# Kernel optimization log

Hardware: AMD Instinct MI355X
Metric: run time of the kernel (lower is better)

## Reference

```python
import jax, jax.numpy as jnp
import numpy as np

N, E, B = 100000, 3200000, 1024
D_LM, K, H, C, L = 1024, 128, 256, 40, 2
T = 0.1
LN_EPS = 1e-5


def _layernorm(x, g, b):
    m = x.mean(-1, keepdims=True)
    v = ((x - m) ** 2).mean(-1, keepdims=True)
    return (x - m) * jax.lax.rsqrt(v + LN_EPS) * g + b


def _gcn_conv(x, W, b, src, dst, norm, self_w):
    h = x @ W
    agg = jax.ops.segment_sum(h[src] * norm[:, None], dst, num_segments=N)
    return agg + h * self_w[:, None] + b


def setup_inputs() -> dict:
    key = jax.random.key(0)
    ks = jax.random.split(key, 20)
    s = 0.02
    rn = lambda k, shp: jax.random.normal(k, shp, jnp.float32) * s
    return {
        "hidden_embeds": jax.random.normal(ks[0], (L, N, D_LM), jnp.float32),
        "proj_W1": rn(ks[1], (L, D_LM, K)),
        "proj_b1": jnp.zeros((L, K), jnp.float32),
        "ln_g": jnp.ones((L, K), jnp.float32),
        "ln_b": jnp.zeros((L, K), jnp.float32),
        "proj_W2": rn(ks[2], (L, K, K)),
        "proj_b2": jnp.zeros((L, K), jnp.float32),
        "alphas": jnp.zeros((L,), jnp.float32),
        "gcn_W1": rn(ks[3], (L, K, H)),
        "gcn_b1": jnp.zeros((L, H), jnp.float32),
        "gcn_W2": rn(ks[4], (L, H, K)),
        "gcn_b2": jnp.zeros((L, K), jnp.float32),
        "clf_W": rn(ks[5], (2 * K, C)),
        "clf_b": jnp.zeros((C,), jnp.float32),
        "edge_index": jax.random.randint(ks[6], (2, E), 0, N, jnp.int64 if jax.config.jax_enable_x64 else jnp.int32),
        "mapping": jax.random.randint(ks[7], (B,), 0, N, jnp.int64 if jax.config.jax_enable_x64 else jnp.int32),
    }


def reference(hidden_embeds, proj_W1, proj_b1, ln_g, ln_b, proj_W2, proj_b2,
              alphas, gcn_W1, gcn_b1, gcn_W2, gcn_b2, clf_W, clf_b,
              edge_index, mapping):
    src, dst = edge_index[0], edge_index[1]
    ones = jnp.ones((E,), jnp.float32)
    # GCN normalization (self loops included): deg over dst + 1
    deg = jax.ops.segment_sum(ones, dst, num_segments=N) + 1.0
    dis = jax.lax.rsqrt(deg)
    norm = dis[src] * dis[dst]          # per-edge D^-1/2 A D^-1/2
    self_w = 1.0 / deg                  # self-loop weight dis[i]*dis[i]

    last = None
    for i in range(L):
        # projector: Linear -> LayerNorm -> ReLU -> Linear
        h = hidden_embeds[i] @ proj_W1[i] + proj_b1[i]
        h = jax.nn.relu(_layernorm(h, ln_g[i], ln_b[i]))
        h = h @ proj_W2[i] + proj_b2[i]
        if i > 0:
            a = jax.nn.sigmoid(alphas[i] / T)
            h = h * a + last * (1.0 - a)
        # 2-layer GCN encoder (dropout=0)
        z = jax.nn.relu(_gcn_conv(h, gcn_W1[i], gcn_b1[i], src, dst, norm, self_w))
        last = _gcn_conv(z, gcn_W2[i], gcn_b2[i], src, dst, norm, self_w)

    # custom_global_mean_pool: mean over {node} U {out-neighbors} U {in-neighbors}
    sum_n = (jax.ops.segment_sum(last[dst], src, num_segments=N)
             + jax.ops.segment_sum(last[src], dst, num_segments=N))
    cnt = (jax.ops.segment_sum(ones, src, num_segments=N)
           + jax.ops.segment_sum(ones, dst, num_segments=N))
    pooled = (last[mapping] + sum_n[mapping]) / (1.0 + cnt[mapping])[:, None]

    out = jnp.concatenate([last[mapping], pooled], axis=1)  # [B, 2K]
    return out @ clf_W + clf_b
```

## Files before the change

### kernel.cpp

```cpp
#include <hip/hip_runtime.h>
#include <hip/hip_bf16.h>
#include <math.h>

using short8 = __attribute__((ext_vector_type(8))) short;
using f32x4  = __attribute__((ext_vector_type(4))) float;

#define PSTRIDE 2048

__device__ __forceinline__ short f2bf(float f) {
    __hip_bfloat16 h = __float2bfloat16(f);
    return *reinterpret_cast<short*>(&h);
}
__device__ __forceinline__ float bf2f(unsigned short u) {
    return __uint_as_float(((unsigned)u) << 16);
}


__global__ void map_scatter_k(const int* __restrict__ mapping, int* __restrict__ map_idx, int B)
{
    int b = blockIdx.x * blockDim.x + threadIdx.x;
    if (b < B) map_idx[mapping[b]] = b;
}

__launch_bounds__(1024)
__global__ void bin_count_k(const int* __restrict__ dst, int E, int* __restrict__ bin_cnt)
{
    __shared__ int h[4096];
    for (int i = threadIdx.x; i < 4096; i += 1024) h[i] = 0;
    __syncthreads();
    int base = blockIdx.x * 32768;
#pragma unroll
    for (int i = 0; i < 32; ++i) {
        int e = base + i * 1024 + threadIdx.x;
        if (e < E) atomicAdd(&h[dst[e] >> 5], 1);
    }
    __syncthreads();
    for (int i = threadIdx.x; i < 4096; i += 1024) {
        int c = h[i];
        if (c) atomicAdd(&bin_cnt[i], c);
    }
}

__launch_bounds__(1024)
__global__ void scan_bins_k(const int* __restrict__ cnt, int* __restrict__ off,
                            int* __restrict__ cur)
{
    __shared__ int wsum[16];
    int tid = threadIdx.x, lane = tid & 63, wid = tid >> 6;
    int4 v = ((const int4*)cnt)[tid];
    int s0 = v.x, s1 = s0 + v.y, s2 = s1 + v.z, s3 = s2 + v.w;
    int q = s3;
#pragma unroll
    for (int o = 1; o < 64; o <<= 1) { int t = __shfl_up(q, o); if (lane >= o) q += t; }
    if (lane == 63) wsum[wid] = q;
    __syncthreads();
    if (wid == 0) {
        int w = (lane < 16) ? wsum[lane] : 0;
#pragma unroll
        for (int o = 1; o < 16; o <<= 1) { int t = __shfl_up(w, o); if (lane >= o) w += t; }
        if (lane < 16) wsum[lane] = w;
    }
    __syncthreads();
    int base = (wid ? wsum[wid - 1] : 0) + q - s3;
    int4 o4; o4.x = base; o4.y = base + s0; o4.z = base + s1; o4.w = base + s2;
    ((int4*)off)[tid] = o4;
    ((int4*)cur)[tid] = o4;
    if (tid == 1023) off[4096] = base + s3;
}

__launch_bounds__(256)
__global__ void bin_scatter_k(const int* __restrict__ ei, int E,
                              const int* __restrict__ map_idx,
                              int* __restrict__ bin_cur, unsigned* __restrict__ pairs,
                              int* __restrict__ pcnt, int* __restrict__ pnb)
{
    int e = blockIdx.x * blockDim.x + threadIdx.x;
    if (e >= E) return;
    int s = ei[e];
    int d = ei[E + e];
    int p = atomicAdd(&bin_cur[d >> 5], 1);
    pairs[p] = (unsigned)s | ((unsigned)(d & 31) << 27);
    int ms = map_idx[s];
    if (ms >= 0) {
        int i = atomicAdd(&pcnt[ms], 1);
        if (i < PSTRIDE) pnb[ms * PSTRIDE + i] = d;
    }
    int md = map_idx[d];
    if (md >= 0) {
        int i = atomicAdd(&pcnt[md], 1);
        if (i < PSTRIDE) pnb[md * PSTRIDE + i] = s;
    }
}

__launch_bounds__(256)
__global__ void bin_csr_k(const unsigned* __restrict__ pairs, const int* __restrict__ bin_off,
                          int* __restrict__ csr_in, int* __restrict__ in_off,
                          float* __restrict__ dis, int N)
{
    __shared__ int lcnt[32];
    __shared__ int lofs[32];
    __shared__ int lcur[32];
    int b = blockIdx.x;
    int tid = threadIdx.x;
    if (tid < 32) lcnt[tid] = 0;
    __syncthreads();
    int beg = bin_off[b], end = bin_off[b + 1];
    for (int i = beg + tid; i < end; i += 256)
        atomicAdd(&lcnt[pairs[i] >> 27], 1);
    __syncthreads();
    if (tid == 0) {
        int run = beg;
#pragma unroll
        for (int j = 0; j < 32; ++j) { lofs[j] = run; lcur[j] = run; run += lcnt[j]; }
    }
    __syncthreads();
    int n0 = b * 32;
    if (tid < 32 && n0 + tid < N) {
        in_off[n0 + tid] = lofs[tid];
        float dg = (float)lcnt[tid] + 1.0f;
        dis[n0 + tid] = rsqrtf(dg);
    }
    if (b == gridDim.x - 1 && tid == 0) in_off[N] = end;
    for (int i = beg + tid; i < end; i += 256) {
        unsigned pr = pairs[i];
        int p = atomicAdd(&lcur[pr >> 27], 1);
        csr_in[p] = (int)(pr & 0x07FFFFFFu);
    }
}

__global__ void transpose_wb_k(const float* __restrict__ src, short* __restrict__ dst,
                               int LAY, int R, int Cc)
{
    int idx = blockIdx.x * blockDim.x + threadIdx.x;
    int tot = LAY * R * Cc;
    if (idx >= tot) return;
    int lay = idx / (R * Cc);
    int rem = idx - lay * R * Cc;
    int r = rem / Cc;
    int c = rem - r * Cc;
    dst[(size_t)lay * R * Cc + (size_t)c * R + r] = f2bf(src[idx]);
}

__launch_bounds__(256)
__global__ void proj_fused_k(const float* __restrict__ X,
                             const short* __restrict__ W1t,
                             const float* __restrict__ b1,
                             const float* __restrict__ lng,
                             const float* __restrict__ lnb,
                             const short* __restrict__ W2t,
                             const float* __restrict__ b2,
                             const float* __restrict__ alphas, int layer,
                             const unsigned short* __restrict__ last,
                             const float* __restrict__ dis,
                             short* __restrict__ out, int nrows)
{
    __shared__ short S[26624];

    const int tid  = threadIdx.x;
    const int lane = tid & 63;
    const int wave = tid >> 6;
    const int wr   = wave >> 1;
    const int wc   = wave & 1;
    const int g    = lane >> 4;
    const int lr   = lane & 15;
    const int row0 = blockIdx.x * 128;

    f32x4 acc[4][4];
#pragma unroll
    for (int fr = 0; fr < 4; ++fr)
#pragma unroll
        for (int fc = 0; fc < 4; ++fc) acc[fr][fc] = (f32x4){0.f, 0.f, 0.f, 0.f};

    const int xr   = tid >> 1;
    const int xc0  = (tid & 1) * 32;
    const bool xvalid = (row0 + xr) < nrows;
    const float* xbase = X + (size_t)(row0 + xr) * 1024 + xc0;
    const short* wbase = W1t + (size_t)(tid >> 1) * 1024 + (tid & 1) * 32;

    float4 xv[8];
    short8 wv[4];
    if (xvalid) {
#pragma unroll
        for (int m = 0; m < 8; ++m) xv[m] = *(const float4*)&xbase[m * 4];
    } else {
#pragma unroll
        for (int m = 0; m < 8; ++m) xv[m] = make_float4(0.f, 0.f, 0.f, 0.f);
    }
#pragma unroll
    for (int m = 0; m < 4; ++m) wv[m] = *(const short8*)&wbase[m * 8];

    for (int k0 = 0; k0 < 1024; k0 += 64) {
#pragma unroll
        for (int m = 0; m < 4; ++m) {
            short8 p;
            p[0]=f2bf(xv[2*m].x); p[1]=f2bf(xv[2*m].y); p[2]=f2bf(xv[2*m].z); p[3]=f2bf(xv[2*m].w);
            p[4]=f2bf(xv[2*m+1].x); p[5]=f2bf(xv[2*m+1].y); p[6]=f2bf(xv[2*m+1].z); p[7]=f2bf(xv[2*m+1].w);
            *(short8*)&S[xr * 72 + xc0 + m * 8] = p;
        }
#pragma unroll
        for (int m = 0; m < 4; ++m)
            *(short8*)&S[9216 + (tid >> 1) * 72 + (tid & 1) * 32 + m * 8] = wv[m];
        __syncthreads();

        if (k0 + 64 < 1024) {
            if (xvalid) {
                const float* xp = xbase + k0 + 64;
#pragma unroll
                for (int m = 0; m < 8; ++m) xv[m] = *(const float4*)&xp[m * 4];
            }
            const short* wp = wbase + k0 + 64;
#pragma unroll
            for (int m = 0; m < 4; ++m) wv[m] = *(const short8*)&wp[m * 8];
        }

#pragma unroll
        for (int kk = 0; kk < 64; kk += 32) {
            short8 a[4], b[4];
#pragma unroll
            for (int fr = 0; fr < 4; ++fr)
                a[fr] = *(short8*)&S[(wr * 64 + fr * 16 + lr) * 72 + kk + g * 8];
#pragma unroll
            for (int fc = 0; fc < 4; ++fc)
                b[fc] = *(short8*)&S[9216 + (wc * 64 + fc * 16 + lr) * 72 + kk + g * 8];
#pragma unroll
            for (int fr = 0; fr < 4; ++fr)
#pragma unroll
                for (int fc = 0; fc < 4; ++fc)
                    acc[fr][fc] = __builtin_amdgcn_mfma_f32_16x16x32_bf16(a[fr], b[fc], acc[fr][fc], 0, 0, 0);
        }
        __syncthreads();
    }

    float* P = (float*)&S[17408];
    {
        float b1v[4], gv[4], bv[4];
#pragma unroll
        for (int fc = 0; fc < 4; ++fc) {
            int col = wc * 64 + fc * 16 + lr;
            b1v[fc] = b1[col]; gv[fc] = lng[col]; bv[fc] = lnb[col];
        }
#pragma unroll
        for (int fr = 0; fr < 4; ++fr) {
#pragma unroll
            for (int j = 0; j < 4; ++j) {
                float s = 0.f, q = 0.f;
#pragma unroll
                for (int fc = 0; fc < 4; ++fc) {
                    float t = acc[fr][fc][j] + b1v[fc];
                    acc[fr][fc][j] = t;
                    s += t; q += t * t;
                }
#pragma unroll
                for (int m = 1; m < 16; m <<= 1) {
                    s += __shfl_xor(s, m);
                    q += __shfl_xor(q, m);
                }
                if (lr == 0) {
                    int row = wr * 64 + fr * 16 + 4 * g + j;
                    P[row * 4 + wc * 2]     = s;
                    P[row * 4 + wc * 2 + 1] = q;
                }
            }
        }
        __syncthreads();
#pragma unroll
        for (int fr = 0; fr < 4; ++fr) {
#pragma unroll
            for (int j = 0; j < 4; ++j) {
                int row = wr * 64 + fr * 16 + 4 * g + j;
                float s = P[row * 4 + 0] + P[row * 4 + 2];
                float q = P[row * 4 + 1] + P[row * 4 + 3];
                float mean = s * (1.0f / 128.0f);
                float var  = q * (1.0f / 128.0f) - mean * mean;
                float inv  = rsqrtf(var + 1e-5f);
#pragma unroll
                for (int fc = 0; fc < 4; ++fc) {
                    float h = fmaxf((acc[fr][fc][j] - mean) * inv * gv[fc] + bv[fc], 0.f);
                    S[row * 136 + wc * 64 + fc * 16 + lr] = f2bf(h);
                }
            }
        }
    }
    __syncthreads();

    f32x4 acc2[4][4];
#pragma unroll
    for (int fr = 0; fr < 4; ++fr)
#pragma unroll
        for (int fc = 0; fc < 4; ++fc) acc2[fr][fc] = (f32x4){0.f, 0.f, 0.f, 0.f};

    for (int k0 = 0; k0 < 128; k0 += 64) {
        {
            int c  = tid >> 1;
            int kb = (tid & 1) * 32;
            const short* wp = W2t + (size_t)c * 128 + k0 + kb;
#pragma unroll
            for (int m = 0; m < 4; ++m)
                *(short8*)&S[17408 + c * 72 + kb + m * 8] = *(const short8*)&wp[m * 8];
        }
        __syncthreads();
#pragma unroll
        for (int kk = 0; kk < 64; kk += 32) {
            short8 a[4], b[4];
#pragma unroll
            for (int fr = 0; fr < 4; ++fr)
                a[fr] = *(short8*)&S[(wr * 64 + fr * 16 + lr) * 136 + k0 + kk + g * 8];
#pragma unroll
            for (int fc = 0; fc < 4; ++fc)
                b[fc] = *(short8*)&S[17408 + (wc * 64 + fc * 16 + lr) * 72 + kk + g * 8];
#pragma unroll
            for (int fr = 0; fr < 4; ++fr)
#pragma unroll
                for (int fc = 0; fc < 4; ++fc)
                    acc2[fr][fc] = __builtin_amdgcn_mfma_f32_16x16x32_bf16(a[fr], b[fc], acc2[fr][fc], 0, 0, 0);
        }
        __syncthreads();
    }

    float b2v[4];
#pragma unroll
    for (int fc = 0; fc < 4; ++fc) b2v[fc] = b2[wc * 64 + fc * 16 + lr];
    float asig = 0.f, omas = 0.f;
    if (last) {
        float al = alphas[layer];
        asig = 1.0f / (1.0f + expf(-al * 10.0f));
        omas = 1.0f - asig;
    }
#pragma unroll
    for (int fr = 0; fr < 4; ++fr) {
#pragma unroll
        for (int j = 0; j < 4; ++j) {
            int gr = row0 + wr * 64 + fr * 16 + 4 * g + j;
            if (gr >= nrows) continue;
            float disr = dis[gr];
#pragma unroll
            for (int fc = 0; fc < 4; ++fc) {
                int col = wc * 64 + fc * 16 + lr;
                float o = acc2[fr][fc][j] + b2v[fc];
                if (last) o = asig * o + omas * bf2f(last[(size_t)gr * 128 + col]);
                out[(size_t)gr * 128 + col] = f2bf(o * disr);
            }
        }
    }
}

__launch_bounds__(256)
__global__ void gcn_mlp_k(const short* __restrict__ U,
                          const short* __restrict__ W1t,
                          const float* __restrict__ gb1,
                          const short* __restrict__ W2t,
                          const float* __restrict__ dis,
                          short* __restrict__ V, int M)
{
    __shared__ short S[35840];

    const int tid  = threadIdx.x;
    const int lane = tid & 63;
    const int wave = tid >> 6;
    const int g    = lane >> 4;
    const int lr   = lane & 15;
    const int m0   = blockIdx.x * 64;

#pragma unroll
    for (int it = 0; it < 4; ++it) {
        int i = tid + it * 256;
        int r = i >> 4;
        int c8 = i & 15;
        short8 v = {0,0,0,0,0,0,0,0};
        int gr = m0 + r;
        if (gr < M) v = *(const short8*)&U[(size_t)gr * 128 + c8 * 8];
        *(short8*)&S[r * 136 + c8 * 8] = v;
    }

    f32x4 acc[4][4];
#pragma unroll
    for (int fr = 0; fr < 4; ++fr)
#pragma unroll
        for (int fc = 0; fc < 4; ++fc) acc[fr][fc] = (f32x4){0.f, 0.f, 0.f, 0.f};

    for (int k0 = 0; k0 < 128; k0 += 64) {
#pragma unroll
        for (int it = 0; it < 8; ++it) {
            int i = tid + it * 256;
            int r = i >> 3;
            int c8 = i & 7;
            *(short8*)&S[17408 + r * 72 + c8 * 8] =
                *(const short8*)&W1t[(size_t)r * 128 + k0 + c8 * 8];
        }
        __syncthreads();
#pragma unroll
        for (int kk = 0; kk < 64; kk += 32) {
            short8 a[4], b[4];
#pragma unroll
            for (int fr = 0; fr < 4; ++fr)
                a[fr] = *(short8*)&S[(fr * 16 + lr) * 136 + k0 + kk + g * 8];
#pragma unroll
            for (int fc = 0; fc < 4; ++fc)
                b[fc] = *(short8*)&S[17408 + (wave * 64 + fc * 16 + lr) * 72 + kk + g * 8];
#pragma unroll
            for (int fr = 0; fr < 4; ++fr)
#pragma unroll
                for (int fc = 0; fc < 4; ++fc)
                    acc[fr][fc] = __builtin_amdgcn_mfma_f32_16x16x32_bf16(a[fr], b[fc], acc[fr][fc], 0, 0, 0);
        }
        __syncthreads();
    }

    {
        float bb[4];
#pragma unroll
        for (int fc = 0; fc < 4; ++fc) bb[fc] = gb1[wave * 64 + fc * 16 + lr];
#pragma unroll
        for (int fr = 0; fr < 4; ++fr) {
#pragma unroll
            for (int j = 0; j < 4; ++j) {
                int rloc = fr * 16 + 4 * g + j;
#pragma unroll
                for (int fc = 0; fc < 4; ++fc) {
                    float zv = fmaxf(acc[fr][fc][j] + bb[fc], 0.f);
                    S[rloc * 264 + wave * 64 + fc * 16 + lr] = f2bf(zv);
                }
            }
        }
    }

    f32x4 acc2[4][2];
#pragma unroll
    for (int fr = 0; fr < 4; ++fr) {
        acc2[fr][0] = (f32x4){0.f, 0.f, 0.f, 0.f};
        acc2[fr][1] = (f32x4){0.f, 0.f, 0.f, 0.f};
    }

    for (int k0 = 0; k0 < 256; k0 += 64) {
#pragma unroll
        for (int it = 0; it < 4; ++it) {
            int i = tid + it * 256;
            int r = i >> 3;
            int c8 = i & 7;
            *(short8*)&S[16896 + r * 72 + c8 * 8] =
                *(const short8*)&W2t[(size_t)r * 256 + k0 + c8 * 8];
        }
        __syncthreads();
#pragma unroll
        for (int kk = 0; kk < 64; kk += 32) {
            short8 a[4], b[2];
#pragma unroll
            for (int fr = 0; fr < 4; ++fr)
                a[fr] = *(short8*)&S[(fr * 16 + lr) * 264 + k0 + kk + g * 8];
#pragma unroll
            for (int fc = 0; fc < 2; ++fc)
                b[fc] = *(short8*)&S[16896 + (wave * 32 + fc * 16 + lr) * 72 + kk + g * 8];
#pragma unroll
            for (int fr = 0; fr < 4; ++fr)
#pragma unroll
                for (int fc = 0; fc < 2; ++fc)
                    acc2[fr][fc] = __builtin_amdgcn_mfma_f32_16x16x32_bf16(a[fr], b[fc], acc2[fr][fc], 0, 0, 0);
        }
        __syncthreads();
    }

#pragma unroll
    for (int fr = 0; fr < 4; ++fr) {
#pragma unroll
        for (int j = 0; j < 4; ++j) {
            int gr = m0 + fr * 16 + 4 * g + j;
            if (gr >= M) continue;
            float disr = dis[gr];
#pragma unroll
            for (int fc = 0; fc < 2; ++fc)
                V[(size_t)gr * 128 + wave * 32 + fc * 16 + lr] = f2bf(acc2[fr][fc][j] * disr);
        }
    }
}

__launch_bounds__(256)
__global__ void agg_k(const unsigned* __restrict__ x, unsigned* __restrict__ y,
                      const int* __restrict__ off, const int* __restrict__ csr,
                      const float* __restrict__ dis,
                      const float* __restrict__ bias, int N)
{
    int node = __builtin_amdgcn_readfirstlane(blockIdx.x * 4 + (threadIdx.x >> 6));
    if (node >= N) return;
    int lane = threadIdx.x & 63;
    int beg = off[node], end = off[node + 1];

    float ax0 = 0.f, ay0 = 0.f, ax1 = 0.f, ay1 = 0.f;
    float ax2 = 0.f, ay2 = 0.f, ax3 = 0.f, ay3 = 0.f;
    int e = beg;
    for (; e + 4 <= end; e += 4) {
        int s0 = csr[e], s1 = csr[e + 1], s2 = csr[e + 2], s3 = csr[e + 3];
        unsigned v0 = x[(size_t)s0 * 64 + lane];
        unsigned v1 = x[(size_t)s1 * 64 + lane];
        unsigned v2 = x[(size_t)s2 * 64 + lane];
        unsigned v3 = x[(size_t)s3 * 64 + lane];
        ax0 += __uint_as_float(v0 << 16);
        ay0 += __uint_as_float(v0 & 0xFFFF0000u);
        ax1 += __uint_as_float(v1 << 16);
        ay1 += __uint_as_float(v1 & 0xFFFF0000u);
        ax2 += __uint_as_float(v2 << 16);
        ay2 += __uint_as_float(v2 & 0xFFFF0000u);
        ax3 += __uint_as_float(v3 << 16);
        ay3 += __uint_as_float(v3 & 0xFFFF0000u);
    }
    for (; e < end; ++e) {
        int s = csr[e];
        unsigned v = x[(size_t)s * 64 + lane];
        ax0 += __uint_as_float(v << 16);
        ay0 += __uint_as_float(v & 0xFFFF0000u);
    }
    unsigned vo = x[(size_t)node * 64 + lane];
    float accx = ((ax0 + ax1) + (ax2 + ax3)) + __uint_as_float(vo << 16);
    float accy = ((ay0 + ay1) + (ay2 + ay3)) + __uint_as_float(vo & 0xFFFF0000u);

    float dn = dis[node];
    float rx = dn * accx;
    float ry = dn * accy;
    if (bias) { rx += bias[lane * 2]; ry += bias[lane * 2 + 1]; }
    unsigned p = (unsigned)(unsigned short)f2bf(rx) | ((unsigned)(unsigned short)f2bf(ry) << 16);
    y[(size_t)node * 64 + lane] = p;
}

__launch_bounds__(128)
__global__ void pool_clf_k(const unsigned short* __restrict__ last,
                           const int* __restrict__ mapping,
                           const int* __restrict__ map_idx,
                           const int* __restrict__ pcnt, const int* __restrict__ pnb,
                           const float* __restrict__ clfW, const float* __restrict__ clfb,
                           float* __restrict__ out, int C)
{
    int b = blockIdx.x;
    int tid = threadIdx.x;
    int n = mapping[b];
    int rep = map_idx[n];
    int cnt = pcnt[rep];
    int m = cnt < PSTRIDE ? cnt : PSTRIDE;

    float s = 0.f;
    const int* nb = pnb + (size_t)rep * PSTRIDE;
    for (int i = 0; i < m; ++i)
        s += bf2f(last[(size_t)nb[i] * 128 + tid]);

    float lv = bf2f(last[(size_t)n * 128 + tid]);
    float pooled = (lv + s) / (1.0f + (float)cnt);

    __shared__ float feat[256];
    feat[tid] = lv;
    feat[128 + tid] = pooled;
    __syncthreads();

    for (int c = tid; c < C; c += blockDim.x) {
        float o = clfb[c];
        for (int j = 0; j < 256; ++j) o = fmaf(feat[j], clfW[j * C + c], o);
        out[(size_t)b * C + c] = o;
    }
}

extern "C" void kernel_launch(void* const* d_in, const int* in_sizes, int n_in,
                              void* d_out, int out_size, void* d_ws, size_t ws_size,
                              hipStream_t stream)
{
    const float* hidden = (const float*)d_in[0];
    const float* pW1    = (const float*)d_in[1];
    const float* pb1    = (const float*)d_in[2];
    const float* lng    = (const float*)d_in[3];
    const float* lnb    = (const float*)d_in[4];
    const float* pW2    = (const float*)d_in[5];
    const float* pb2    = (const float*)d_in[6];
    const float* alphas = (const float*)d_in[7];
    const float* gW1    = (const float*)d_in[8];
    const float* gb1    = (const float*)d_in[9];
    const float* gW2    = (const float*)d_in[10];
    const float* gb2    = (const float*)d_in[11];
    const float* clfW   = (const float*)d_in[12];
    const float* clfb   = (const float*)d_in[13];
    const int*   ei     = (const int*)d_in[14];
    const int*   mapping= (const int*)d_in[15];

    const int L   = in_sizes[7];
    const int K   = in_sizes[2] / L;
    const int H   = in_sizes[9] / L;
    const int C   = in_sizes[13];
    const int DLM = in_sizes[1] / (L * K);
    const int N   = in_sizes[0] / (L * DLM);
    const int E   = in_sizes[14] / 2;
    const int B   = in_sizes[15];
    const int NBINS = (N + 31) / 32;

    char* ws = (char*)d_ws;
    size_t off = 0;
    auto carve = [&](size_t bytes) -> char* {
        char* p = ws + off;
        off += (bytes + 255) & ~(size_t)255;
        return p;
    };
    int*      map_idx = (int*)carve((size_t)N * 4);
    int*      pcnt    = (int*)carve((size_t)B * 4);
    int*      pnb     = (int*)carve((size_t)B * PSTRIDE * 4);
    int*      bin_cnt = (int*)carve(4096 * 4);
    int*      bin_off = (int*)carve(4097 * 4);
    int*      bin_cur = (int*)carve(4096 * 4);
    unsigned* pairs   = (unsigned*)carve((size_t)E * 4);
    int*      in_off  = (int*)carve((size_t)(N + 1) * 4);
    float*    dis     = (float*)carve((size_t)N * 4);
    int*      csr_in  = (int*)carve((size_t)E * 4);
    short*    bufA    = (short*)carve((size_t)N * K * 2);
    short*    bufU    = (short*)carve((size_t)N * K * 2);
    short*    bufLast = (short*)carve((size_t)N * K * 2);
    short*    w1t     = (short*)carve((size_t)L * K * DLM * 2);
    short*    w2t     = (short*)carve((size_t)L * K * K * 2);
    short*    gw1t    = (short*)carve((size_t)L * H * K * 2);
    short*    gw2t    = (short*)carve((size_t)L * K * H * 2);
    (void)ws_size; (void)n_in; (void)out_size;

    hipMemsetAsync(bin_cnt, 0, 4096 * 4, stream);
    hipMemsetAsync(map_idx, 0xFF, (size_t)N * 4, stream);
    hipMemsetAsync(pcnt, 0, (size_t)B * 4, stream);
    map_scatter_k<<<dim3((B + 255) / 256), 256, 0, stream>>>(mapping, map_idx, B);
    bin_count_k<<<dim3((E + 32767) / 32768), 1024, 0, stream>>>(ei + E, E, bin_cnt);
    scan_bins_k<<<dim3(1), 1024, 0, stream>>>(bin_cnt, bin_off, bin_cur);
    bin_scatter_k<<<dim3((E + 255) / 256), 256, 0, stream>>>(ei, E, map_idx, bin_cur,
                                                             pairs, pcnt, pnb);
    bin_csr_k<<<dim3(NBINS), 256, 0, stream>>>(pairs, bin_off, csr_in, in_off,
                                               dis, N);

    transpose_wb_k<<<dim3((L * DLM * K + 255) / 256), 256, 0, stream>>>(pW1, w1t, L, DLM, K);
    transpose_wb_k<<<dim3((L * K * K + 255) / 256), 256, 0, stream>>>(pW2, w2t, L, K, K);
    transpose_wb_k<<<dim3((L * K * H + 255) / 256), 256, 0, stream>>>(gW1, gw1t, L, K, H);
    transpose_wb_k<<<dim3((L * H * K + 255) / 256), 256, 0, stream>>>(gW2, gw2t, L, H, K);

    const int nblk64  = (N + 63) / 64;
    const int nblk128 = (N + 127) / 128;

    for (int i = 0; i < L; ++i) {
        proj_fused_k<<<dim3(nblk128), 256, 0, stream>>>(
            hidden + (size_t)i * N * DLM,
            w1t + (size_t)i * K * DLM,
            pb1 + (size_t)i * K,
            lng + (size_t)i * K,
            lnb + (size_t)i * K,
            w2t + (size_t)i * K * K,
            pb2 + (size_t)i * K,
            alphas, i,
            (i > 0) ? (const unsigned short*)bufLast : nullptr,
            dis,
            bufA, N);

        agg_k<<<dim3((N + 3) / 4), 256, 0, stream>>>(
            (const unsigned*)bufA, (unsigned*)bufU, in_off, csr_in, dis, nullptr, N);
        gcn_mlp_k<<<dim3(nblk64), 256, 0, stream>>>(
            bufU, gw1t + (size_t)i * H * K, gb1 + (size_t)i * H,
            gw2t + (size_t)i * K * H, dis, bufA, N);
        agg_k<<<dim3((N + 3) / 4), 256, 0, stream>>>(
            (const unsigned*)bufA, (unsigned*)bufLast, in_off, csr_in, dis,
            gb2 + (size_t)i * K, N);
    }

    pool_clf_k<<<dim3(B), 128, 0, stream>>>((const unsigned short*)bufLast,
                                            mapping, map_idx, pcnt, pnb,
                                            clfW, clfb, (float*)d_out, C);
}
```

Baseline: 1.206 ms.

## Raise projector kernel occupancy by dropping register prefetch and shrinking LDS

```diff
diff --git a/kernel.cpp b/kernel.cpp
--- a/kernel.cpp
+++ b/kernel.cpp
@@ -141,7 +141,7 @@
     dst[(size_t)lay * R * Cc + (size_t)c * R + r] = f2bf(src[idx]);
 }
 
-__launch_bounds__(256)
+__launch_bounds__(256, 4)
 __global__ void proj_fused_k(const float* __restrict__ X,
                              const short* __restrict__ W1t,
                              const float* __restrict__ b1,
@@ -154,7 +154,7 @@
                              const float* __restrict__ dis,
                              short* __restrict__ out, int nrows)
 {
-    __shared__ short S[26624];
+    __shared__ short S[18432];
 
     const int tid  = threadIdx.x;
     const int lane = tid & 63;
@@ -177,42 +177,33 @@
     const float* xbase = X + (size_t)(row0 + xr) * 1024 + xc0;
     const short* wbase = W1t + (size_t)(tid >> 1) * 1024 + (tid & 1) * 32;
 
-    float4 xv[8];
-    short8 wv[4];
-    if (xvalid) {
-#pragma unroll
-        for (int m = 0; m < 8; ++m) xv[m] = *(const float4*)&xbase[m * 4];
-    } else {
-#pragma unroll
-        for (int m = 0; m < 8; ++m) xv[m] = make_float4(0.f, 0.f, 0.f, 0.f);
-    }
-#pragma unroll
-    for (int m = 0; m < 4; ++m) wv[m] = *(const short8*)&wbase[m * 8];
-
     for (int k0 = 0; k0 < 1024; k0 += 64) {
-#pragma unroll
-        for (int m = 0; m < 4; ++m) {
-            short8 p;
-            p[0]=f2bf(xv[2*m].x); p[1]=f2bf(xv[2*m].y); p[2]=f2bf(xv[2*m].z); p[3]=f2bf(xv[2*m].w);
-            p[4]=f2bf(xv[2*m+1].x); p[5]=f2bf(xv[2*m+1].y); p[6]=f2bf(xv[2*m+1].z); p[7]=f2bf(xv[2*m+1].w);
-            *(short8*)&S[xr * 72 + xc0 + m * 8] = p;
-        }
-#pragma unroll
-        for (int m = 0; m < 4; ++m)
-            *(short8*)&S[9216 + (tid >> 1) * 72 + (tid & 1) * 32 + m * 8] = wv[m];
+        {
+            float4 v[8];
+            if (xvalid) {
+                const float* xp = xbase + k0;
+#pragma unroll
+                for (int m = 0; m < 8; ++m) v[m] = *(const float4*)&xp[m * 4];
+            } else {
+#pragma unroll
+                for (int m = 0; m < 8; ++m) v[m] = make_float4(0.f, 0.f, 0.f, 0.f);
+            }
+#pragma unroll
+            for (int m = 0; m < 4; ++m) {
+                short8 p;
+                p[0]=f2bf(v[2*m].x); p[1]=f2bf(v[2*m].y); p[2]=f2bf(v[2*m].z); p[3]=f2bf(v[2*m].w);
+                p[4]=f2bf(v[2*m+1].x); p[5]=f2bf(v[2*m+1].y); p[6]=f2bf(v[2*m+1].z); p[7]=f2bf(v[2*m+1].w);
+                *(short8*)&S[xr * 72 + xc0 + m * 8] = p;
+            }
+        }
+        {
+            const short* wp = wbase + k0;
+#pragma unroll
+            for (int m = 0; m < 4; ++m)
+                *(short8*)&S[9216 + (tid >> 1) * 72 + (tid & 1) * 32 + m * 8] =
+                    *(const short8*)&wp[m * 8];
+        }
         __syncthreads();
-
-        if (k0 + 64 < 1024) {
-            if (xvalid) {
-                const float* xp = xbase + k0 + 64;
-#pragma unroll
-                for (int m = 0; m < 8; ++m) xv[m] = *(const float4*)&xp[m * 4];
-            }
-            const short* wp = wbase + k0 + 64;
-#pragma unroll
-            for (int m = 0; m < 4; ++m) wv[m] = *(const short8*)&wp[m * 8];
-        }
-
 #pragma unroll
         for (int kk = 0; kk < 64; kk += 32) {
             short8 a[4], b[4];
@@ -289,32 +280,25 @@
 #pragma unroll
         for (int fc = 0; fc < 4; ++fc) acc2[fr][fc] = (f32x4){0.f, 0.f, 0.f, 0.f};
 
-    for (int k0 = 0; k0 < 128; k0 += 64) {
-        {
-            int c  = tid >> 1;
-            int kb = (tid & 1) * 32;
-            const short* wp = W2t + (size_t)c * 128 + k0 + kb;
-#pragma unroll
-            for (int m = 0; m < 4; ++m)
-                *(short8*)&S[17408 + c * 72 + kb + m * 8] = *(const short8*)&wp[m * 8];
-        }
-        __syncthreads();
-#pragma unroll
-        for (int kk = 0; kk < 64; kk += 32) {
-            short8 a[4], b[4];
-#pragma unroll
-            for (int fr = 0; fr < 4; ++fr)
-                a[fr] = *(short8*)&S[(wr * 64 + fr * 16 + lr) * 136 + k0 + kk + g * 8];
+    const short* w2base[4];
+#pragma unroll
+    for (int fc = 0; fc < 4; ++fc)
+        w2base[fc] = W2t + (size_t)(wc * 64 + fc * 16 + lr) * 128 + g * 8;
+
+#pragma unroll
+    for (int k0 = 0; k0 < 128; k0 += 32) {
+        short8 a[4], b[4];
+#pragma unroll
+        for (int fc = 0; fc < 4; ++fc)
+            b[fc] = *(const short8*)&w2base[fc][k0];
+#pragma unroll
+        for (int fr = 0; fr < 4; ++fr)
+            a[fr] = *(short8*)&S[(wr * 64 + fr * 16 + lr) * 136 + k0 + g * 8];
+#pragma unroll
+        for (int fr = 0; fr < 4; ++fr)
 #pragma unroll
             for (int fc = 0; fc < 4; ++fc)
-                b[fc] = *(short8*)&S[17408 + (wc * 64 + fc * 16 + lr) * 72 + kk + g * 8];
-#pragma unroll
-            for (int fr = 0; fr < 4; ++fr)
-#pragma unroll
-                for (int fc = 0; fc < 4; ++fc)
-                    acc2[fr][fc] = __builtin_amdgcn_mfma_f32_16x16x32_bf16(a[fr], b[fc], acc2[fr][fc], 0, 0, 0);
-        }
-        __syncthreads();
+                acc2[fr][fc] = __builtin_amdgcn_mfma_f32_16x16x32_bf16(a[fr], b[fc], acc2[fr][fc], 0, 0, 0);
     }
 
     float b2v[4];
```

Measured after the change: 1.207 ms. About the same (+0.1%).
